# Performance work log

Measured on AMD Instinct MI355X. Metric: run time of the kernel, lower is better.

Reference implementation:

```python
import jax, jax.numpy as jnp
import numpy as np

EPS = 1e-5  # PyTorch BatchNorm1d default eps


def setup_inputs() -> dict:
    key = jax.random.key(0)
    ks = jax.random.split(key, 16)
    M, B, S, H = 2, 4, 2048, 4096
    HID, INT = 256, 128  # head_hidden_dim, head_hidden_dim // 2
    randn = lambda k, shape, scale=1.0: jax.random.normal(k, shape, jnp.float32) * scale
    return {
        'h': randn(ks[0], (M, B, S, H)),
        'w1': randn(ks[1], (M, HID, H), 0.02),
        'b1': randn(ks[2], (M, HID), 0.02),
        'g1': jax.random.uniform(ks[3], (M, HID), jnp.float32, 0.5, 1.5),
        'be1': randn(ks[4], (M, HID), 0.02),
        'm1': randn(ks[5], (M, HID), 0.1),
        'v1': jax.random.uniform(ks[6], (M, HID), jnp.float32, 0.5, 1.5),
        'w2': randn(ks[7], (M, INT, HID), 0.05),
        'b2': randn(ks[8], (M, INT), 0.02),
        'g2': jax.random.uniform(ks[9], (M, INT), jnp.float32, 0.5, 1.5),
        'be2': randn(ks[10], (M, INT), 0.02),
        'm2': randn(ks[11], (M, INT), 0.1),
        'v2': jax.random.uniform(ks[12], (M, INT), jnp.float32, 0.5, 1.5),
        'w3': randn(ks[13], (M, 1, INT), 0.05),
        'b3': randn(ks[14], (M, 1), 0.02),
    }


def _bn_eval(x, gamma, beta, mean, var):
    # eval-mode BatchNorm1d over the feature axis; per-model params broadcast
    # x: [M,B,S,K]; params: [M,K]
    inv = gamma * jax.lax.rsqrt(var + EPS)  # [M,K]
    return x * inv[:, None, None, :] + (beta - mean * inv)[:, None, None, :]


def reference(h, w1, b1, g1, be1, m1, v1, w2, b2, g2, be2, m2, v2, w3, b3):
    # Vectorized equivalent of the per-position Python loop applying each
    # model's ScalarProjectionHead to every token representation.
    x = jnp.einsum('mbsh,mkh->mbsk', h, w1) + b1[:, None, None, :]   # [M,B,S,256]
    x = jax.nn.relu(_bn_eval(x, g1, be1, m1, v1))                     # dropout = identity (eval)
    x = jnp.einsum('mbsk,mjk->mbsj', x, w2) + b2[:, None, None, :]   # [M,B,S,128]
    x = jax.nn.relu(_bn_eval(x, g2, be2, m2, v2))
    s = jnp.einsum('mbsj,moj->mbso', x, w3) + b3[:, None, None, :]   # [M,B,S,1]
    # stack per-model scores along last dim, as torch.stack(..., dim=-1)
    all_raw_scores = jnp.transpose(s[..., 0], (1, 2, 0))             # [B,S,M]
    return all_raw_scores
```

## Files before the change

kernel.cpp:

```cpp
#include <hip/hip_runtime.h>
#include <hip/hip_bf16.h>

#define EPSF 1e-5f

typedef __attribute__((ext_vector_type(8))) short bf16x8;
typedef __attribute__((ext_vector_type(4))) float f32x4;
typedef __attribute__((ext_vector_type(4))) unsigned int u32x4;

__device__ __forceinline__ unsigned short f2bf(float f) {
  union { float f; unsigned u; } v; v.f = f;
  unsigned r = v.u + 0x7fffu + ((v.u >> 16) & 1u);
  return (unsigned short)(r >> 16);
}

__device__ __forceinline__ u32x4 cvtpk8(f32x4 a, f32x4 b) {
  u32x4 r;
  asm("v_cvt_pk_bf16_f32 %0, %1, %2" : "=v"(r[0]) : "v"(a[0]), "v"(a[1]));
  asm("v_cvt_pk_bf16_f32 %0, %1, %2" : "=v"(r[1]) : "v"(a[2]), "v"(a[3]));
  asm("v_cvt_pk_bf16_f32 %0, %1, %2" : "=v"(r[2]) : "v"(b[0]), "v"(b[1]));
  asm("v_cvt_pk_bf16_f32 %0, %1, %2" : "=v"(r[3]) : "v"(b[2]), "v"(b[3]));
  return r;
}

__global__ void prep_kernel(const float* __restrict__ w1, const float* __restrict__ b1,
                            const float* __restrict__ g1, const float* __restrict__ be1,
                            const float* __restrict__ m1, const float* __restrict__ v1,
                            const float* __restrict__ w2, const float* __restrict__ b2,
                            const float* __restrict__ g2, const float* __restrict__ be2,
                            const float* __restrict__ m2, const float* __restrict__ v2,
                            unsigned short* __restrict__ w1p, unsigned short* __restrict__ w2f,
                            float* __restrict__ bias1, float* __restrict__ bias2) {
  int idx = blockIdx.x * blockDim.x + threadIdx.x;
  int stride = gridDim.x * blockDim.x;
  for (int i = idx; i < 262144; i += stride) {
    int l  = i & 63;
    int f  = (i >> 6) & 7;
    int kt = (i >> 9) & 63;
    int c  = (i >> 15) & 3;
    int m  = i >> 17;
    int st = f >> 2, j = f & 3;
    int n  = c * 64 + j * 16 + (l & 15);
    int k0 = kt * 64 + st * 32 + (l >> 4) * 8;
    int mn = m * 256 + n;
    float inv = g1[mn] * rsqrtf(v1[mn] + EPSF);
    const float* src = w1 + (size_t)mn * 4096 + k0;
    unsigned short* dst = w1p + (size_t)i * 8;
#pragma unroll
    for (int e = 0; e < 8; ++e) dst[e] = f2bf(src[e] * inv);
  }
  for (int i = idx; i < 2 * 128 * 256; i += stride) {
    int mj = i >> 8;
    float inv = g2[mj] * rsqrtf(v2[mj] + EPSF);
    w2f[i] = f2bf(w2[i] * inv);
  }
  if (idx < 512) {
    float inv = g1[idx] * rsqrtf(v1[idx] + EPSF);
    bias1[idx] = b1[idx] * inv + be1[idx] - m1[idx] * inv;
  }
  if (idx < 256) {
    float inv = g2[idx] * rsqrtf(v2[idx] + EPSF);
    bias2[idx] = b2[idx] * inv + be2[idx] - m2[idx] * inv;
  }
}

#define BLOAD(BN, KT)                                                  \
  {                                                                    \
    BN[0] = *(const bf16x8*)(pB + (size_t)(KT) * 8192 + 0 * 1024);     \
    BN[1] = *(const bf16x8*)(pB + (size_t)(KT) * 8192 + 1 * 1024);     \
    BN[2] = *(const bf16x8*)(pB + (size_t)(KT) * 8192 + 2 * 1024);     \
    BN[3] = *(const bf16x8*)(pB + (size_t)(KT) * 8192 + 3 * 1024);     \
    BN[4] = *(const bf16x8*)(pB + (size_t)(KT) * 8192 + 4 * 1024);     \
    BN[5] = *(const bf16x8*)(pB + (size_t)(KT) * 8192 + 5 * 1024);     \
    BN[6] = *(const bf16x8*)(pB + (size_t)(KT) * 8192 + 6 * 1024);     \
    BN[7] = *(const bf16x8*)(pB + (size_t)(KT) * 8192 + 7 * 1024);     \
  }

#define ALOAD(AR, KOFF)                                                \
  {                                                                    \
    AR[0] = *(const f32x4*)(aSrc + (KOFF));                            \
    AR[1] = *(const f32x4*)(aSrc + (KOFF) + 4);                        \
    AR[2] = *(const f32x4*)(aSrc + (KOFF) + 8);                        \
    AR[3] = *(const f32x4*)(aSrc + (KOFF) + 12);                       \
  }

#define AWRITE(AR, DBASE)                                              \
  {                                                                    \
    u32x4 lo_ = cvtpk8(AR[0], AR[1]);                                  \
    u32x4 hi_ = cvtpk8(AR[2], AR[3]);                                  \
    *(u32x4*)((DBASE) + aOff0) = lo_;                                  \
    *(u32x4*)((DBASE) + aOff1) = hi_;                                  \
  }

#define AFREAD(ABUF)                                                   \
  {                                                                    \
    _Pragma("unroll") for (int st = 0; st < 2; ++st)                   \
    _Pragma("unroll") for (int i = 0; i < 4; ++i) {                    \
      int row_ = i * 16 + l15;                                         \
      int g_ = st * 4 + lq;                                            \
      aF[st][i] = *(const bf16x8*)((ABUF) + row_ * 128 + ((g_ ^ (row_ & 7)) << 4)); \
    }                                                                  \
  }

#define MFMA16(BC)                                                     \
  {                                                                    \
    _Pragma("unroll") for (int st = 0; st < 2; ++st)                   \
    _Pragma("unroll") for (int i = 0; i < 4; ++i)                      \
    _Pragma("unroll") for (int j = 0; j < 4; ++j)                      \
      acc[i][j] = __builtin_amdgcn_mfma_f32_16x16x32_bf16(aF[st][i], BC[st * 4 + j], acc[i][j], 0, 0, 0); \
  }

#define BOUNDARY()                                                     \
  __builtin_amdgcn_sched_barrier(0x77);                                \
  asm volatile("s_waitcnt lgkmcnt(0)");                                \
  __builtin_amdgcn_s_barrier();                                        \
  __builtin_amdgcn_sched_barrier(0x77);

__global__ __launch_bounds__(256) void fused_heads_kernel(
    const float* __restrict__ h,
    const unsigned short* __restrict__ w1p,
    const unsigned short* __restrict__ w2f,
    const float* __restrict__ bias1,
    const float* __restrict__ bias2,
    const float* __restrict__ w3,
    const float* __restrict__ b3,
    float* __restrict__ out) {
  __shared__ __align__(16) char lds[33792];

  const int tid = threadIdx.x;
  const int lane = tid & 63;
  const int wv = tid >> 6;
  const int l15 = lane & 15;
  const int lq = lane >> 4;

  const int bid = blockIdx.x;
  const int mdl = (bid >> 2) & 1;
  const int rb = (bid >> 3) * 4 + (bid & 3);

  const float* hM = h + ((size_t)mdl * 8192 + (size_t)rb * 64) * 4096;
  const char* pB = (const char*)w1p + (size_t)(mdl * 4 + wv) * 524288 + lane * 16;

  const int arow = tid >> 2;
  const int akseg = tid & 3;
  const float* aSrc = hM + (size_t)arow * 4096 + akseg * 16;
  const int ax = arow & 7;
  const int aOff0 = arow * 128 + (((akseg * 2) ^ ax) << 4);
  const int aOff1 = arow * 128 + (((akseg * 2 + 1) ^ ax) << 4);

  f32x4 acc[4][4];
#pragma unroll
  for (int i = 0; i < 4; ++i)
#pragma unroll
    for (int j = 0; j < 4; ++j)
#pragma unroll
      for (int q = 0; q < 4; ++q) acc[i][j][q] = 0.f;

  bf16x8 bb0[8], bb1[8];
  f32x4 aR0[4], aR1[4];
  bf16x8 aF[2][4];

  char* const Ab0 = lds;
  char* const Ab1 = lds + 8192;

  ALOAD(aR0, 0)
  BLOAD(bb0, 0)
  ALOAD(aR1, 64)
  AWRITE(aR0, Ab0)
  BOUNDARY()

#pragma unroll 1
  for (int kt2 = 0; kt2 < 31; ++kt2) {
    const int kt = kt2 * 2;
    AFREAD(Ab0)
    BLOAD(bb1, kt + 1)
    ALOAD(aR0, (kt + 2) * 64)
    MFMA16(bb0)
    AWRITE(aR1, Ab1)
    BOUNDARY()
    AFREAD(Ab1)
    BLOAD(bb0, kt + 2)
    ALOAD(aR1, (kt + 3) * 64)
    MFMA16(bb1)
    AWRITE(aR0, Ab0)
    BOUNDARY()
  }
  AFREAD(Ab0)
  BLOAD(bb1, 63)
  MFMA16(bb0)
  AWRITE(aR1, Ab1)
  BOUNDARY()
  AFREAD(Ab1)
  MFMA16(bb1)
  BOUNDARY()

  float b1v[4];
#pragma unroll
  for (int j = 0; j < 4; ++j) b1v[j] = bias1[mdl * 256 + wv * 64 + j * 16 + l15];
#pragma unroll
  for (int i = 0; i < 4; ++i) {
#pragma unroll
    for (int j = 0; j < 4; ++j) {
      int n = wv * 64 + j * 16 + l15;
#pragma unroll
      for (int q = 0; q < 4; ++q) {
        int row = i * 16 + lq * 4 + q;
        float x = fmaxf(acc[i][j][q] + b1v[j], 0.f);
        *(unsigned short*)(lds + row * 512 + ((((n >> 3) ^ (row & 7)) << 4) | ((n & 7) << 1))) = f2bf(x);
      }
    }
  }
  __syncthreads();

  f32x4 acc2[4][2];
#pragma unroll
  for (int i = 0; i < 4; ++i)
#pragma unroll
    for (int j = 0; j < 2; ++j)
#pragma unroll
      for (int q = 0; q < 4; ++q) acc2[i][j][q] = 0.f;

  const unsigned short* w2m = w2f + mdl * (128 * 256);
#pragma unroll
  for (int st = 0; st < 8; ++st) {
    int k8 = st * 32 + lq * 8;
    bf16x8 aX[4], bW[2];
#pragma unroll
    for (int i = 0; i < 4; ++i) {
      int row = i * 16 + l15;
      aX[i] = *(const bf16x8*)(lds + row * 512 + ((((k8 >> 3) ^ (row & 7)) << 4)));
    }
#pragma unroll
    for (int j = 0; j < 2; ++j) {
      int n2 = wv * 32 + j * 16 + l15;
      bW[j] = *(const bf16x8*)(w2m + n2 * 256 + k8);
    }
#pragma unroll
    for (int i = 0; i < 4; ++i)
#pragma unroll
      for (int j = 0; j < 2; ++j)
        acc2[i][j] = __builtin_amdgcn_mfma_f32_16x16x32_bf16(aX[i], bW[j], acc2[i][j], 0, 0, 0);
  }

  float w3v[2], b2v[2];
#pragma unroll
  for (int j = 0; j < 2; ++j) {
    int n2 = wv * 32 + j * 16 + l15;
    w3v[j] = w3[mdl * 128 + n2];
    b2v[j] = bias2[mdl * 128 + n2];
  }
  float* part = (float*)(lds + 32768);
#pragma unroll
  for (int i = 0; i < 4; ++i) {
#pragma unroll
    for (int q = 0; q < 4; ++q) {
      float val = 0.f;
#pragma unroll
      for (int j = 0; j < 2; ++j) {
        float x = fmaxf(acc2[i][j][q] + b2v[j], 0.f);
        val += x * w3v[j];
      }
#pragma unroll
      for (int mk = 1; mk < 16; mk <<= 1) val += __shfl_xor(val, mk, 64);
      if (l15 == 0) part[wv * 64 + i * 16 + lq * 4 + q] = val;
    }
  }
  __syncthreads();
  if (tid < 64) {
    float s = part[tid] + part[64 + tid] + part[128 + tid] + part[192 + tid] + b3[mdl];
    out[((size_t)(rb * 64 + tid)) * 2 + mdl] = s;
  }
}

extern "C" void kernel_launch(void* const* d_in, const int* in_sizes, int n_in,
                              void* d_out, int out_size, void* d_ws, size_t ws_size,
                              hipStream_t stream) {
  const float* h   = (const float*)d_in[0];
  const float* w1  = (const float*)d_in[1];
  const float* b1  = (const float*)d_in[2];
  const float* g1  = (const float*)d_in[3];
  const float* be1 = (const float*)d_in[4];
  const float* m1  = (const float*)d_in[5];
  const float* v1  = (const float*)d_in[6];
  const float* w2  = (const float*)d_in[7];
  const float* b2  = (const float*)d_in[8];
  const float* g2  = (const float*)d_in[9];
  const float* be2 = (const float*)d_in[10];
  const float* m2  = (const float*)d_in[11];
  const float* v2  = (const float*)d_in[12];
  const float* w3  = (const float*)d_in[13];
  const float* b3  = (const float*)d_in[14];

  char* ws = (char*)d_ws;
  unsigned short* w1p = (unsigned short*)ws;
  unsigned short* w2f = (unsigned short*)(ws + 4194304);
  float* bias1 = (float*)(ws + 4325376);
  float* bias2 = (float*)(ws + 4327424);

  prep_kernel<<<1024, 256, 0, stream>>>(w1, b1, g1, be1, m1, v1,
                                        w2, b2, g2, be2, m2, v2,
                                        w1p, w2f, bias1, bias2);
  fused_heads_kernel<<<256, 256, 0, stream>>>(h, w1p, w2f, bias1, bias2, w3, b3,
                                              (float*)d_out);
}
```

Before: 77.91 us.

## Triple-buffer LDS A tiles and double-buffer A fragments in main GEMM loop

Changes the K-loop pipeline from two LDS A buffers to three rotating buffers, with A fragments read from LDS one step ahead into alternating register sets. Global loads are issued one more stage ahead, and the loop is unrolled six-way to cover the rotation. The aim is to hide LDS-read and global-load latency behind MFMA work. The cost is many more live registers; launch bounds are set to one block per SM, which may reduce occupancy or cause spills.

```diff
diff --git a/kernel.cpp b/kernel.cpp
--- a/kernel.cpp
+++ b/kernel.cpp
@@ -91,22 +91,22 @@
     *(u32x4*)((DBASE) + aOff1) = hi_;                                  \
   }
 
-#define AFREAD(ABUF)                                                   \
+#define AFREAD2(AF, ABUF)                                              \
   {                                                                    \
     _Pragma("unroll") for (int st = 0; st < 2; ++st)                   \
     _Pragma("unroll") for (int i = 0; i < 4; ++i) {                    \
       int row_ = i * 16 + l15;                                         \
       int g_ = st * 4 + lq;                                            \
-      aF[st][i] = *(const bf16x8*)((ABUF) + row_ * 128 + ((g_ ^ (row_ & 7)) << 4)); \
+      AF[st][i] = *(const bf16x8*)((ABUF) + row_ * 128 + ((g_ ^ (row_ & 7)) << 4)); \
     }                                                                  \
   }
 
-#define MFMA16(BC)                                                     \
+#define MFMA16(AF, BC)                                                 \
   {                                                                    \
     _Pragma("unroll") for (int st = 0; st < 2; ++st)                   \
     _Pragma("unroll") for (int i = 0; i < 4; ++i)                      \
     _Pragma("unroll") for (int j = 0; j < 4; ++j)                      \
-      acc[i][j] = __builtin_amdgcn_mfma_f32_16x16x32_bf16(aF[st][i], BC[st * 4 + j], acc[i][j], 0, 0, 0); \
+      acc[i][j] = __builtin_amdgcn_mfma_f32_16x16x32_bf16(AF[st][i], BC[st * 4 + j], acc[i][j], 0, 0, 0); \
   }
 
 #define BOUNDARY()                                                     \
@@ -115,7 +115,15 @@
   __builtin_amdgcn_s_barrier();                                        \
   __builtin_amdgcn_sched_barrier(0x77);
 
-__global__ __launch_bounds__(256) void fused_heads_kernel(
+#define STEP_FULL(KT, ABR, ABW, BBC, BBN, ARC, ARN, AFC, AFN)          \
+  AFREAD2(AFN, ABR)                                                    \
+  BLOAD(BBN, (KT) + 1)                                                 \
+  ALOAD(ARN, ((KT) + 3) * 64)                                          \
+  MFMA16(AFC, BBC)                                                     \
+  AWRITE(ARC, ABW)                                                     \
+  BOUNDARY()
+
+__global__ __launch_bounds__(256, 1) void fused_heads_kernel(
     const float* __restrict__ h,
     const unsigned short* __restrict__ w1p,
     const unsigned short* __restrict__ w2f,
@@ -156,40 +164,42 @@
 
   bf16x8 bb0[8], bb1[8];
   f32x4 aR0[4], aR1[4];
-  bf16x8 aF[2][4];
+  bf16x8 aFA[2][4], aFB[2][4];
 
   char* const Ab0 = lds;
   char* const Ab1 = lds + 8192;
+  char* const Ab2 = lds + 16384;
 
   ALOAD(aR0, 0)
   BLOAD(bb0, 0)
   ALOAD(aR1, 64)
   AWRITE(aR0, Ab0)
-  BOUNDARY()
+  AWRITE(aR1, Ab1)
+  ALOAD(aR0, 128)
+  BOUNDARY()
+  AFREAD2(aFA, Ab0)
 
 #pragma unroll 1
-  for (int kt2 = 0; kt2 < 31; ++kt2) {
-    const int kt = kt2 * 2;
-    AFREAD(Ab0)
-    BLOAD(bb1, kt + 1)
-    ALOAD(aR0, (kt + 2) * 64)
-    MFMA16(bb0)
-    AWRITE(aR1, Ab1)
-    BOUNDARY()
-    AFREAD(Ab1)
-    BLOAD(bb0, kt + 2)
-    ALOAD(aR1, (kt + 3) * 64)
-    MFMA16(bb1)
-    AWRITE(aR0, Ab0)
-    BOUNDARY()
-  }
-  AFREAD(Ab0)
+  for (int t = 0; t < 10; ++t) {
+    const int kt = t * 6;
+    STEP_FULL(kt + 0, Ab1, Ab2, bb0, bb1, aR0, aR1, aFA, aFB)
+    STEP_FULL(kt + 1, Ab2, Ab0, bb1, bb0, aR1, aR0, aFB, aFA)
+    STEP_FULL(kt + 2, Ab0, Ab1, bb0, bb1, aR0, aR1, aFA, aFB)
+    STEP_FULL(kt + 3, Ab1, Ab2, bb1, bb0, aR1, aR0, aFB, aFA)
+    STEP_FULL(kt + 4, Ab2, Ab0, bb0, bb1, aR0, aR1, aFA, aFB)
+    STEP_FULL(kt + 5, Ab0, Ab1, bb1, bb0, aR1, aR0, aFB, aFA)
+  }
+  STEP_FULL(60, Ab1, Ab2, bb0, bb1, aR0, aR1, aFA, aFB)
+  AFREAD2(aFA, Ab2)
+  BLOAD(bb0, 62)
+  MFMA16(aFB, bb1)
+  AWRITE(aR1, Ab0)
+  BOUNDARY()
+  AFREAD2(aFB, Ab0)
   BLOAD(bb1, 63)
-  MFMA16(bb0)
-  AWRITE(aR1, Ab1)
-  BOUNDARY()
-  AFREAD(Ab1)
-  MFMA16(bb1)
+  MFMA16(aFA, bb0)
+  BOUNDARY()
+  MFMA16(aFB, bb1)
   BOUNDARY()
 
   float b1v[4];
```

After: 87.77 us. 1.13x slower.

## Split each block's work across eight waves instead of four

Applied to the files above, without the earlier changes.

Doubles the block size to 512 threads. Each wave now computes a 64x32 slice of the first GEMM instead of 64x64, and 16 columns instead of 32 of the second GEMM. Per-thread A loads and B fragment loads are halved, and the final reduction sums eight partials. The aim is more latency hiding per CU and less register pressure per wave, at the cost of more redundant A-fragment LDS reads across waves and more barrier participants.

```diff
diff --git a/kernel.cpp b/kernel.cpp
--- a/kernel.cpp
+++ b/kernel.cpp
@@ -65,30 +65,22 @@
 
 #define BLOAD(BN, KT)                                                  \
   {                                                                    \
-    BN[0] = *(const bf16x8*)(pB + (size_t)(KT) * 8192 + 0 * 1024);     \
-    BN[1] = *(const bf16x8*)(pB + (size_t)(KT) * 8192 + 1 * 1024);     \
-    BN[2] = *(const bf16x8*)(pB + (size_t)(KT) * 8192 + 2 * 1024);     \
-    BN[3] = *(const bf16x8*)(pB + (size_t)(KT) * 8192 + 3 * 1024);     \
-    BN[4] = *(const bf16x8*)(pB + (size_t)(KT) * 8192 + 4 * 1024);     \
-    BN[5] = *(const bf16x8*)(pB + (size_t)(KT) * 8192 + 5 * 1024);     \
-    BN[6] = *(const bf16x8*)(pB + (size_t)(KT) * 8192 + 6 * 1024);     \
-    BN[7] = *(const bf16x8*)(pB + (size_t)(KT) * 8192 + 7 * 1024);     \
+    BN[0] = *(const bf16x8*)(pB + (size_t)(KT) * 8192 + 0);            \
+    BN[1] = *(const bf16x8*)(pB + (size_t)(KT) * 8192 + 1024);         \
+    BN[2] = *(const bf16x8*)(pB + (size_t)(KT) * 8192 + 4096);         \
+    BN[3] = *(const bf16x8*)(pB + (size_t)(KT) * 8192 + 5120);         \
   }
 
 #define ALOAD(AR, KOFF)                                                \
   {                                                                    \
     AR[0] = *(const f32x4*)(aSrc + (KOFF));                            \
     AR[1] = *(const f32x4*)(aSrc + (KOFF) + 4);                        \
-    AR[2] = *(const f32x4*)(aSrc + (KOFF) + 8);                        \
-    AR[3] = *(const f32x4*)(aSrc + (KOFF) + 12);                       \
   }
 
 #define AWRITE(AR, DBASE)                                              \
   {                                                                    \
-    u32x4 lo_ = cvtpk8(AR[0], AR[1]);                                  \
-    u32x4 hi_ = cvtpk8(AR[2], AR[3]);                                  \
-    *(u32x4*)((DBASE) + aOff0) = lo_;                                  \
-    *(u32x4*)((DBASE) + aOff1) = hi_;                                  \
+    u32x4 w_ = cvtpk8(AR[0], AR[1]);                                   \
+    *(u32x4*)((DBASE) + aOff) = w_;                                    \
   }
 
 #define AFREAD(ABUF)                                                   \
@@ -101,12 +93,12 @@
     }                                                                  \
   }
 
-#define MFMA16(BC)                                                     \
+#define MFMA8(BC)                                                      \
   {                                                                    \
     _Pragma("unroll") for (int st = 0; st < 2; ++st)                   \
     _Pragma("unroll") for (int i = 0; i < 4; ++i)                      \
-    _Pragma("unroll") for (int j = 0; j < 4; ++j)                      \
-      acc[i][j] = __builtin_amdgcn_mfma_f32_16x16x32_bf16(aF[st][i], BC[st * 4 + j], acc[i][j], 0, 0, 0); \
+    _Pragma("unroll") for (int j = 0; j < 2; ++j)                      \
+      acc[i][j] = __builtin_amdgcn_mfma_f32_16x16x32_bf16(aF[st][i], BC[st * 2 + j], acc[i][j], 0, 0, 0); \
   }
 
 #define BOUNDARY()                                                     \
@@ -115,7 +107,7 @@
   __builtin_amdgcn_s_barrier();                                        \
   __builtin_amdgcn_sched_barrier(0x77);
 
-__global__ __launch_bounds__(256) void fused_heads_kernel(
+__global__ __launch_bounds__(512) void fused_heads_kernel(
     const float* __restrict__ h,
     const unsigned short* __restrict__ w1p,
     const unsigned short* __restrict__ w2f,
@@ -124,7 +116,7 @@
     const float* __restrict__ w3,
     const float* __restrict__ b3,
     float* __restrict__ out) {
-  __shared__ __align__(16) char lds[33792];
+  __shared__ __align__(16) char lds[34816];
 
   const int tid = threadIdx.x;
   const int lane = tid & 63;
@@ -137,25 +129,24 @@
   const int rb = (bid >> 3) * 4 + (bid & 3);
 
   const float* hM = h + ((size_t)mdl * 8192 + (size_t)rb * 64) * 4096;
-  const char* pB = (const char*)w1p + (size_t)(mdl * 4 + wv) * 524288 + lane * 16;
-
-  const int arow = tid >> 2;
-  const int akseg = tid & 3;
-  const float* aSrc = hM + (size_t)arow * 4096 + akseg * 16;
-  const int ax = arow & 7;
-  const int aOff0 = arow * 128 + (((akseg * 2) ^ ax) << 4);
-  const int aOff1 = arow * 128 + (((akseg * 2 + 1) ^ ax) << 4);
-
-  f32x4 acc[4][4];
+  const char* pB = (const char*)w1p + (size_t)(mdl * 4 + (wv >> 1)) * 524288
+                   + (wv & 1) * 2048 + lane * 16;
+
+  const int arow = tid >> 3;
+  const int akseg = tid & 7;
+  const float* aSrc = hM + (size_t)arow * 4096 + akseg * 8;
+  const int aOff = arow * 128 + ((akseg ^ (arow & 7)) << 4);
+
+  f32x4 acc[4][2];
 #pragma unroll
   for (int i = 0; i < 4; ++i)
 #pragma unroll
-    for (int j = 0; j < 4; ++j)
+    for (int j = 0; j < 2; ++j)
 #pragma unroll
       for (int q = 0; q < 4; ++q) acc[i][j][q] = 0.f;
 
-  bf16x8 bb0[8], bb1[8];
-  f32x4 aR0[4], aR1[4];
+  bf16x8 bb0[4], bb1[4];
+  f32x4 aR0[2], aR1[2];
   bf16x8 aF[2][4];
 
   char* const Ab0 = lds;
@@ -173,33 +164,33 @@
     AFREAD(Ab0)
     BLOAD(bb1, kt + 1)
     ALOAD(aR0, (kt + 2) * 64)
-    MFMA16(bb0)
+    MFMA8(bb0)
     AWRITE(aR1, Ab1)
     BOUNDARY()
     AFREAD(Ab1)
     BLOAD(bb0, kt + 2)
     ALOAD(aR1, (kt + 3) * 64)
-    MFMA16(bb1)
+    MFMA8(bb1)
     AWRITE(aR0, Ab0)
     BOUNDARY()
   }
   AFREAD(Ab0)
   BLOAD(bb1, 63)
-  MFMA16(bb0)
+  MFMA8(bb0)
   AWRITE(aR1, Ab1)
   BOUNDARY()
   AFREAD(Ab1)
-  MFMA16(bb1)
+  MFMA8(bb1)
   BOUNDARY()
 
-  float b1v[4];
-#pragma unroll
-  for (int j = 0; j < 4; ++j) b1v[j] = bias1[mdl * 256 + wv * 64 + j * 16 + l15];
+  float b1v[2];
+#pragma unroll
+  for (int j = 0; j < 2; ++j) b1v[j] = bias1[mdl * 256 + wv * 32 + j * 16 + l15];
 #pragma unroll
   for (int i = 0; i < 4; ++i) {
 #pragma unroll
-    for (int j = 0; j < 4; ++j) {
-      int n = wv * 64 + j * 16 + l15;
+    for (int j = 0; j < 2; ++j) {
+      int n = wv * 32 + j * 16 + l15;
 #pragma unroll
       for (int q = 0; q < 4; ++q) {
         int row = i * 16 + lq * 4 + q;
@@ -210,54 +201,44 @@
   }
   __syncthreads();
 
-  f32x4 acc2[4][2];
+  f32x4 acc2[4];
 #pragma unroll
   for (int i = 0; i < 4; ++i)
 #pragma unroll
-    for (int j = 0; j < 2; ++j)
-#pragma unroll
-      for (int q = 0; q < 4; ++q) acc2[i][j][q] = 0.f;
+    for (int q = 0; q < 4; ++q) acc2[i][q] = 0.f;
 
   const unsigned short* w2m = w2f + mdl * (128 * 256);
 #pragma unroll
   for (int st = 0; st < 8; ++st) {
     int k8 = st * 32 + lq * 8;
-    bf16x8 aX[4], bW[2];
+    bf16x8 aX[4], bW;
 #pragma unroll
     for (int i = 0; i < 4; ++i) {
       int row = i * 16 + l15;
       aX[i] = *(const bf16x8*)(lds + row * 512 + ((((k8 >> 3) ^ (row & 7)) << 4)));
     }
-#pragma unroll
-    for (int j = 0; j < 2; ++j) {
-      int n2 = wv * 32 + j * 16 + l15;
-      bW[j] = *(const bf16x8*)(w2m + n2 * 256 + k8);
+    {
+      int n2 = wv * 16 + l15;
+      bW = *(const bf16x8*)(w2m + n2 * 256 + k8);
     }
 #pragma unroll
     for (int i = 0; i < 4; ++i)
-#pragma unroll
-      for (int j = 0; j < 2; ++j)
-        acc2[i][j] = __builtin_amdgcn_mfma_f32_16x16x32_bf16(aX[i], bW[j], acc2[i][j], 0, 0, 0);
-  }
-
-  float w3v[2], b2v[2];
-#pragma unroll
-  for (int j = 0; j < 2; ++j) {
-    int n2 = wv * 32 + j * 16 + l15;
-    w3v[j] = w3[mdl * 128 + n2];
-    b2v[j] = bias2[mdl * 128 + n2];
+      acc2[i] = __builtin_amdgcn_mfma_f32_16x16x32_bf16(aX[i], bW, acc2[i], 0, 0, 0);
+  }
+
+  float w3v, b2v;
+  {
+    int n2 = wv * 16 + l15;
+    w3v = w3[mdl * 128 + n2];
+    b2v = bias2[mdl * 128 + n2];
   }
   float* part = (float*)(lds + 32768);
 #pragma unroll
   for (int i = 0; i < 4; ++i) {
 #pragma unroll
     for (int q = 0; q < 4; ++q) {
-      float val = 0.f;
-#pragma unroll
-      for (int j = 0; j < 2; ++j) {
-        float x = fmaxf(acc2[i][j][q] + b2v[j], 0.f);
-        val += x * w3v[j];
-      }
+      float x = fmaxf(acc2[i][q] + b2v, 0.f);
+      float val = x * w3v;
 #pragma unroll
       for (int mk = 1; mk < 16; mk <<= 1) val += __shfl_xor(val, mk, 64);
       if (l15 == 0) part[wv * 64 + i * 16 + lq * 4 + q] = val;
@@ -265,7 +246,9 @@
   }
   __syncthreads();
   if (tid < 64) {
-    float s = part[tid] + part[64 + tid] + part[128 + tid] + part[192 + tid] + b3[mdl];
+    float s = part[tid] + part[64 + tid] + part[128 + tid] + part[192 + tid]
+            + part[256 + tid] + part[320 + tid] + part[384 + tid] + part[448 + tid]
+            + b3[mdl];
     out[((size_t)(rb * 64 + tid)) * 2 + mdl] = s;
   }
 }
@@ -298,6 +281,6 @@
   prep_kernel<<<1024, 256, 0, stream>>>(w1, b1, g1, be1, m1, v1,
                                         w2, b2, g2, be2, m2, v2,
                                         w1p, w2f, bias1, bias2);
-  fused_heads_kernel<<<256, 256, 0, stream>>>(h, w1p, w2f, bias1, bias2, w3, b3,
+  fused_heads_kernel<<<256, 512, 0, stream>>>(h, w1p, w2f, bias1, bias2, w3, b3,
                                               (float*)d_out);
 }
```

New measurement: 72.40 us, median of 2. -7.1%, faster.

## Split first GEMM along K into two partial-sum blocks with separate heads kernel

Applied to the files above, without the earlier changes.

Splits the large first GEMM (K=4096) into two halves handled by separate blocks, doubling the grid from 256 to 512 blocks so more of the device's compute units are occupied. Partial fp32 results go to a workspace buffer. A new heads kernel then sums the two partials, adds bias, applies ReLU, converts to bf16 in LDS and runs the remaining layers. This trades extra global traffic (32 MB of fp32 partials written then read) and an additional launch for better parallelism.

```diff
diff --git a/kernel.cpp b/kernel.cpp
--- a/kernel.cpp
+++ b/kernel.cpp
@@ -115,16 +115,11 @@
   __builtin_amdgcn_s_barrier();                                        \
   __builtin_amdgcn_sched_barrier(0x77);
 
-__global__ __launch_bounds__(256) void fused_heads_kernel(
+__global__ __launch_bounds__(256) void gemm1_kernel(
     const float* __restrict__ h,
     const unsigned short* __restrict__ w1p,
-    const unsigned short* __restrict__ w2f,
-    const float* __restrict__ bias1,
-    const float* __restrict__ bias2,
-    const float* __restrict__ w3,
-    const float* __restrict__ b3,
-    float* __restrict__ out) {
-  __shared__ __align__(16) char lds[33792];
+    float* __restrict__ X1p) {
+  __shared__ __align__(16) char lds[16384];
 
   const int tid = threadIdx.x;
   const int lane = tid & 63;
@@ -133,11 +128,14 @@
   const int lq = lane >> 4;
 
   const int bid = blockIdx.x;
-  const int mdl = (bid >> 2) & 1;
-  const int rb = (bid >> 3) * 4 + (bid & 3);
-
-  const float* hM = h + ((size_t)mdl * 8192 + (size_t)rb * 64) * 4096;
-  const char* pB = (const char*)w1p + (size_t)(mdl * 4 + wv) * 524288 + lane * 16;
+  const int kh = bid >> 8;
+  const int b8 = bid & 255;
+  const int mdl = (b8 >> 2) & 1;
+  const int rb = (b8 >> 3) * 4 + (b8 & 3);
+
+  const float* hM = h + ((size_t)mdl * 8192 + (size_t)rb * 64) * 4096 + kh * 2048;
+  const char* pB = (const char*)w1p + (size_t)(mdl * 4 + wv) * 524288
+                   + (size_t)kh * 262144 + lane * 16;
 
   const int arow = tid >> 2;
   const int akseg = tid & 3;
@@ -168,7 +166,7 @@
   BOUNDARY()
 
 #pragma unroll 1
-  for (int kt2 = 0; kt2 < 31; ++kt2) {
+  for (int kt2 = 0; kt2 < 15; ++kt2) {
     const int kt = kt2 * 2;
     AFREAD(Ab0)
     BLOAD(bb1, kt + 1)
@@ -184,17 +182,14 @@
     BOUNDARY()
   }
   AFREAD(Ab0)
-  BLOAD(bb1, 63)
+  BLOAD(bb1, 31)
   MFMA16(bb0)
   AWRITE(aR1, Ab1)
   BOUNDARY()
   AFREAD(Ab1)
   MFMA16(bb1)
-  BOUNDARY()
-
-  float b1v[4];
-#pragma unroll
-  for (int j = 0; j < 4; ++j) b1v[j] = bias1[mdl * 256 + wv * 64 + j * 16 + l15];
+
+  float* Xb = X1p + ((size_t)kh * 16384 + (size_t)mdl * 8192 + (size_t)rb * 64) * 256;
 #pragma unroll
   for (int i = 0; i < 4; ++i) {
 #pragma unroll
@@ -203,9 +198,54 @@
 #pragma unroll
       for (int q = 0; q < 4; ++q) {
         int row = i * 16 + lq * 4 + q;
-        float x = fmaxf(acc[i][j][q] + b1v[j], 0.f);
-        *(unsigned short*)(lds + row * 512 + ((((n >> 3) ^ (row & 7)) << 4) | ((n & 7) << 1))) = f2bf(x);
+        Xb[(size_t)row * 256 + n] = acc[i][j][q];
       }
+    }
+  }
+}
+
+__global__ __launch_bounds__(256) void heads_kernel(
+    const float* __restrict__ X1p,
+    const unsigned short* __restrict__ w2f,
+    const float* __restrict__ bias1,
+    const float* __restrict__ bias2,
+    const float* __restrict__ w3,
+    const float* __restrict__ b3,
+    float* __restrict__ out) {
+  __shared__ __align__(16) char lds[33792];
+
+  const int tid = threadIdx.x;
+  const int lane = tid & 63;
+  const int wv = tid >> 6;
+  const int l15 = lane & 15;
+  const int lq = lane >> 4;
+
+  const int bid = blockIdx.x;
+  const int mdl = (bid >> 2) & 1;
+  const int rb = (bid >> 3) * 4 + (bid & 3);
+
+  {
+    const int r = tid >> 2;
+    const int seg = tid & 3;
+    const float* xp0 = X1p + ((size_t)mdl * 8192 + (size_t)rb * 64 + r) * 256 + seg * 64;
+    const float* xp1 = xp0 + (size_t)16384 * 256;
+    const float* bs = bias1 + mdl * 256 + seg * 64;
+#pragma unroll
+    for (int g = 0; g < 8; ++g) {
+      f32x4 a0 = *(const f32x4*)(xp0 + g * 8);
+      f32x4 a1 = *(const f32x4*)(xp0 + g * 8 + 4);
+      f32x4 c0 = *(const f32x4*)(xp1 + g * 8);
+      f32x4 c1 = *(const f32x4*)(xp1 + g * 8 + 4);
+      f32x4 d0 = *(const f32x4*)(bs + g * 8);
+      f32x4 d1 = *(const f32x4*)(bs + g * 8 + 4);
+#pragma unroll
+      for (int e = 0; e < 4; ++e) {
+        a0[e] = fmaxf(a0[e] + c0[e] + d0[e], 0.f);
+        a1[e] = fmaxf(a1[e] + c1[e] + d1[e], 0.f);
+      }
+      u32x4 w = cvtpk8(a0, a1);
+      int gran = seg * 8 + g;
+      *(u32x4*)(lds + r * 512 + ((gran ^ (r & 7)) << 4)) = w;
     }
   }
   __syncthreads();
@@ -294,10 +334,12 @@
   unsigned short* w2f = (unsigned short*)(ws + 4194304);
   float* bias1 = (float*)(ws + 4325376);
   float* bias2 = (float*)(ws + 4327424);
+  float* X1p   = (float*)(ws + 8388608);
 
   prep_kernel<<<1024, 256, 0, stream>>>(w1, b1, g1, be1, m1, v1,
                                         w2, b2, g2, be2, m2, v2,
                                         w1p, w2f, bias1, bias2);
-  fused_heads_kernel<<<256, 256, 0, stream>>>(h, w1p, w2f, bias1, bias2, w3, b3,
-                                              (float*)d_out);
-}
+  gemm1_kernel<<<512, 256, 0, stream>>>(h, w1p, X1p);
+  heads_kernel<<<256, 256, 0, stream>>>(X1p, w2f, bias1, bias2, w3, b3,
+                                        (float*)d_out);
+}
```

After: 100.5 us. 1.29x slower.
